# Optimization experiments

Measured on AMD Instinct MI355X. Metric: run time of the kernel, lower is better.

The kernel has to match this reference:

```python
import jax, jax.numpy as jnp
import numpy as np

N_WIRES = 12
N_LAYERS = 3
DIM = 2 ** N_WIRES
BATCH = 512


def _rot_matrix(a, b, c):
    """Fused U = RZ(c) @ RY(b) @ RX(a) as a 2x2 complex64 matrix."""
    ca, sa = jnp.cos(a * 0.5), jnp.sin(a * 0.5)
    cb, sb = jnp.cos(b * 0.5), jnp.sin(b * 0.5)
    ec = jnp.exp(-0.5j * c)  # e^{-i c/2}
    zero = jnp.zeros_like(ec)
    RX = jnp.stack([jnp.stack([ca + 0j, -1j * sa]),
                    jnp.stack([-1j * sa, ca + 0j])]).astype(jnp.complex64)
    RY = jnp.stack([jnp.stack([cb, -sb]),
                    jnp.stack([sb, cb])]).astype(jnp.complex64)
    RZ = jnp.stack([jnp.stack([ec, zero]),
                    jnp.stack([zero, jnp.conj(ec)])]).astype(jnp.complex64)
    return RZ @ RY @ RX


def _apply_1q(psi, U, wire):
    B = psi.shape[0]
    dl, dr = 2 ** wire, 2 ** (N_WIRES - wire - 1)
    s = psi.reshape(B, dl, 2, dr)
    s = jnp.einsum('ij,bljr->blir', U, s)
    return s.reshape(B, DIM)


def _apply_cnot_adjacent(psi, wire):
    # CNOT(control=wire, target=wire+1): permute (10 <-> 11) on the joint axis
    B = psi.shape[0]
    dl, dr = 2 ** wire, 2 ** (N_WIRES - wire - 2)
    s = psi.reshape(B, dl, 4, dr)
    s = jnp.take(s, jnp.array([0, 1, 3, 2]), axis=2)
    return s.reshape(B, DIM)


def _circuit(state_batch, weights):
    psi = state_batch.astype(jnp.complex64)  # QubitStateVector init
    for l in range(N_LAYERS):
        for w in range(N_WIRES):
            U = _rot_matrix(weights[l, w, 0], weights[l, w, 1], weights[l, w, 2])
            psi = _apply_1q(psi, U, w)
        for w in range(N_WIRES - 1):  # 'cnot' chain entanglement
            psi = _apply_cnot_adjacent(psi, w)
    B = state_batch.shape[0]
    probs = (psi.real ** 2 + psi.imag ** 2).reshape((B,) + (2,) * N_WIRES)
    feats = []
    for w in range(N_WIRES):  # <Z_w> = p(0) - p(1)
        axes = tuple(a for a in range(1, N_WIRES + 1) if a != w + 1)
        p = probs.sum(axis=axes)  # (B, 2)
        feats.append(p[:, 0] - p[:, 1])
    return jnp.stack(feats, axis=-1)  # (B, N_WIRES)


def setup_inputs() -> dict:
    key = jax.random.key(0)
    k1, k2, k3, k4 = jax.random.split(key, 4)
    state = jax.random.normal(k1, (BATCH, DIM), dtype=jnp.float32)
    state = state / jnp.linalg.norm(state, axis=-1, keepdims=True)  # valid quantum states
    weights = jax.random.uniform(k2, (N_LAYERS, N_WIRES, 3), dtype=jnp.float32,
                                 minval=0.0, maxval=2.0 * np.pi)
    head_w = jax.random.normal(k3, (1, N_WIRES), dtype=jnp.float32) / np.sqrt(N_WIRES)
    head_b = jax.random.normal(k4, (1,), dtype=jnp.float32) * 0.01
    return {"state_batch": state, "weights": weights, "head_w": head_w, "head_b": head_b}


def reference(state_batch, weights, head_w, head_b):
    feats = _circuit(state_batch, weights)          # (B, N_WIRES) PauliZ expvals
    out = feats @ head_w.T + head_b                 # Linear(num_wires, 1)
    return out[:, 0]                                # squeeze(-1) -> (B,)
```

## Files before the change

kernel.cpp:

```cpp
#include <hip/hip_runtime.h>


namespace {

typedef float v2f __attribute__((ext_vector_type(2)));

constexpr int N_WIRES  = 12;
constexpr int DIM      = 1 << N_WIRES;
constexpr int THREADS  = 256;
constexpr int PER      = 16;
constexpr int NGATES   = 36;
constexpr int PADC     = 4606;

__device__ __forceinline__ v2f cmul(v2f u, v2f p) {
    v2f d;
    asm("v_pk_mul_f32 %0, %1, %2 op_sel_hi:[1,0]"
        : "=v"(d) : "v"(p), "v"(u));
    asm("v_pk_fma_f32 %0, %1, %2, %0 op_sel:[1,1,0] op_sel_hi:[0,1,1] neg_lo:[0,1,0]"
        : "+v"(d) : "v"(p), "v"(u));
    return d;
}
__device__ __forceinline__ void cfma(v2f& d, v2f u, v2f p) {
    asm("v_pk_fma_f32 %0, %1, %2, %0 op_sel_hi:[1,0,1]"
        : "+v"(d) : "v"(p), "v"(u));
    asm("v_pk_fma_f32 %0, %1, %2, %0 op_sel:[1,1,0] op_sel_hi:[0,1,1] neg_lo:[0,1,0]"
        : "+v"(d) : "v"(p), "v"(u));
}

__device__ __forceinline__ void apply4(v2f amp[PER], const v2f (*Um)[4], int gbase)
{
    #pragma unroll
    for (int gg = 0; gg < 4; ++gg) {
        const v2f u00 = Um[gbase + gg][0];
        const v2f u01 = Um[gbase + gg][1];
        const v2f u10 = Um[gbase + gg][2];
        const v2f u11 = Um[gbase + gg][3];
        const int st = 8 >> gg;
        #pragma unroll
        for (int k0 = 0; k0 < PER; ++k0) {
            if (k0 & st) continue;
            const int k1 = k0 | st;
            const v2f p = amp[k0], q = amp[k1];
            v2f np = cmul(u00, p); cfma(np, u01, q);
            v2f nq = cmul(u10, p); cfma(nq, u11, q);
            amp[k0] = np;
            amp[k1] = nq;
        }
    }
}

__global__ __launch_bounds__(THREADS, 4)
void qcirc_kernel(const float* __restrict__ state,
                  const float* __restrict__ weights,
                  const float* __restrict__ head_w,
                  const float* __restrict__ head_b,
                  float* __restrict__ out)
{
    __shared__ __align__(16) v2f buf[PADC];
    __shared__ __align__(16) v2f Umat[NGATES][4];
    __shared__ float redbuf[THREADS / 64];

    const int t = threadIdx.x;
    const int b = blockIdx.x;

    if (t < NGATES) {
        const float* wp = weights + t * 3;
        float ha = 0.5f * wp[0], hb = 0.5f * wp[1], hc = 0.5f * wp[2];
        float ca = cosf(ha), sa = sinf(ha);
        float cb = cosf(hb), sb = sinf(hb);
        float ecr = cosf(hc), eci = -sinf(hc);
        float t0 = cb * ca, t1 = sb * sa, t2 = sb * ca, t3 = cb * sa;
        float u00r =  ecr * t0 - eci * t1;
        float u00i =  ecr * t1 + eci * t0;
        float u10r =  ecr * t2 - eci * t3;
        float u10i = -ecr * t3 - eci * t2;
        Umat[t][0] = (v2f){ u00r,  u00i};
        Umat[t][1] = (v2f){-u10r,  u10i};
        Umat[t][2] = (v2f){ u10r,  u10i};
        Umat[t][3] = (v2f){ u00r, -u00i};
    }

    const int T  = t >> 4, u = t & 15;
    const int bA = 18 * T + u;
    const int bB = 288 * T + u;
    const int bC = 18 * t;
    const int tb  = t ^ (t >> 1);
    const int tbx = tb ^ 128;
    const int pb0 = 18 * (tb  >> 4) + (tb  & 15);
    const int pb1 = 18 * (tbx >> 4) + (tbx & 15);

    float hw[N_WIRES];
    #pragma unroll
    for (int w = 0; w < N_WIRES; ++w) hw[w] = head_w[w];
    int it = t ^ (t >> 1); it ^= it >> 2; it ^= it >> 4;
    float chi = 0.f;
    #pragma unroll
    for (int w = 0; w < 8; ++w)
        chi += ((it >> (7 - w)) & 1) ? -hw[w] : hw[w];
    const int parfill = (__popc(t) & 1) ? 0xF : 0;

    v2f amp[PER];
    {
        const float* sp = state + (size_t)b * DIM;
        #pragma unroll
        for (int k = 0; k < PER; ++k)
            amp[k] = (v2f){sp[(k << 8) | t], 0.f};
    }
    __syncthreads();

    #pragma unroll
    for (int l = 0; l < 3; ++l) {
        const int gb = l * 12;
        if (l > 0) {
            #pragma unroll
            for (int k = 0; k < PER; ++k) {
                const int g = k ^ (k >> 1);
                amp[k] = buf[((k & 1) ? pb1 : pb0) + 288 * g];
            }
            __syncthreads();
        }

        apply4(amp, Umat, gb + 0);
        #pragma unroll
        for (int k = 0; k < PER; ++k) buf[bA + 288 * k] = amp[k];
        __syncthreads();

        #pragma unroll
        for (int k = 0; k < PER; ++k) amp[k] = buf[bB + 18 * k];
        apply4(amp, Umat, gb + 4);
        #pragma unroll
        for (int k = 0; k < PER; ++k) buf[bB + 18 * k] = amp[k];
        __syncthreads();

        {
            const float4* r = reinterpret_cast<const float4*>(&buf[bC]);
            #pragma unroll
            for (int k = 0; k < PER / 2; ++k) {
                float4 v = r[k];
                amp[2 * k]     = (v2f){v.x, v.y};
                amp[2 * k + 1] = (v2f){v.z, v.w};
            }
        }
        apply4(amp, Umat, gb + 8);
        if (l < 2) {
            float4* w = reinterpret_cast<float4*>(&buf[bC]);
            #pragma unroll
            for (int k = 0; k < PER / 2; ++k)
                w[k] = make_float4(amp[2 * k].x, amp[2 * k].y,
                                   amp[2 * k + 1].x, amp[2 * k + 1].y);
            __syncthreads();
        }
    }

    float acc = 0.f;
    #pragma unroll
    for (int k = 0; k < PER; ++k) {
        int ml = (k ^ (k >> 1)); ml ^= ml >> 2; ml ^= parfill;
        float c = chi;
        c += ((ml >> 3) & 1) ? -hw[8]  : hw[8];
        c += ((ml >> 2) & 1) ? -hw[9]  : hw[9];
        c += ((ml >> 1) & 1) ? -hw[10] : hw[10];
        c += ( ml       & 1) ? -hw[11] : hw[11];
        float p = amp[k].x * amp[k].x + amp[k].y * amp[k].y;
        acc += p * c;
    }

    #pragma unroll
    for (int off = 32; off > 0; off >>= 1)
        acc += __shfl_down(acc, off, 64);
    if ((t & 63) == 0) redbuf[t >> 6] = acc;
    __syncthreads();
    if (t == 0) {
        float s = 0.f;
        #pragma unroll
        for (int q = 0; q < THREADS / 64; ++q) s += redbuf[q];
        out[b] = s + head_b[0];
    }
}

}

extern "C" void kernel_launch(void* const* d_in, const int* in_sizes, int n_in,
                              void* d_out, int out_size, void* d_ws, size_t ws_size,
                              hipStream_t stream)
{
    const float* state   = (const float*)d_in[0];
    const float* weights = (const float*)d_in[1];
    const float* head_w  = (const float*)d_in[2];
    const float* head_b  = (const float*)d_in[3];
    float* out = (float*)d_out;

    const int batch = in_sizes[0] / DIM;
    qcirc_kernel<<<batch, THREADS, 0, stream>>>(state, weights, head_w, head_b, out);
}
```

Measured before the change: 76.14 us.

## Use 512 threads with 8 amplitudes each and double-buffered LDS

Doubles the thread count per block to 512, so each thread holds 8 amplitudes instead of 16. Each layer now runs four passes of three gates through shared memory instead of three passes of four. The shared buffer is doubled so that consecutive passes alternate between two buffers, which removes one barrier per layer. The aim is more wavefronts to hide latency and fewer registers per thread, at the cost of an extra LDS exchange pass per layer and twice the LDS footprint per block.

Measured after the change: 78.21 us. 2.7% more time.

```diff
diff --git a/kernel.cpp b/kernel.cpp
--- a/kernel.cpp
+++ b/kernel.cpp
@@ -7,8 +7,8 @@
 
 constexpr int N_WIRES  = 12;
 constexpr int DIM      = 1 << N_WIRES;
-constexpr int THREADS  = 256;
-constexpr int PER      = 16;
+constexpr int THREADS  = 512;
+constexpr int PER      = 8;
 constexpr int NGATES   = 36;
 constexpr int PADC     = 4606;
 
@@ -27,15 +27,15 @@
         : "+v"(d) : "v"(p), "v"(u));
 }
 
-__device__ __forceinline__ void apply4(v2f amp[PER], const v2f (*Um)[4], int gbase)
+__device__ __forceinline__ void apply3(v2f amp[PER], const v2f (*Um)[4], int gbase)
 {
     #pragma unroll
-    for (int gg = 0; gg < 4; ++gg) {
+    for (int gg = 0; gg < 3; ++gg) {
         const v2f u00 = Um[gbase + gg][0];
         const v2f u01 = Um[gbase + gg][1];
         const v2f u10 = Um[gbase + gg][2];
         const v2f u11 = Um[gbase + gg][3];
-        const int st = 8 >> gg;
+        const int st = 4 >> gg;
         #pragma unroll
         for (int k0 = 0; k0 < PER; ++k0) {
             if (k0 & st) continue;
@@ -56,7 +56,7 @@
                   const float* __restrict__ head_b,
                   float* __restrict__ out)
 {
-    __shared__ __align__(16) v2f buf[PADC];
+    __shared__ __align__(16) v2f buf[2][PADC];
     __shared__ __align__(16) v2f Umat[NGATES][4];
     __shared__ float redbuf[THREADS / 64];
 
@@ -80,31 +80,37 @@
         Umat[t][3] = (v2f){ u00r, -u00i};
     }
 
-    const int T  = t >> 4, u = t & 15;
-    const int bA = 18 * T + u;
-    const int bB = 288 * T + u;
-    const int bC = 18 * t;
-    const int tb  = t ^ (t >> 1);
-    const int tbx = tb ^ 128;
-    const int pb0 = 18 * (tb  >> 4) + (tb  & 15);
-    const int pb1 = 18 * (tbx >> 4) + (tbx & 15);
+    const int bP0 = 18 * (t >> 4) + (t & 15);
+    const int bP1 = 576 * (t >> 6) + 18 * ((t >> 4) & 3) + (t & 15);
+    const int bP2 = 72 * (t >> 3) + (t & 7);
+    const int bP3 = 18 * (t >> 1) + 8 * (t & 1);
+
+    const int gt = t ^ (t >> 1);
+    const int gl = gt & 15, gh = gt >> 4;
+    int fg[PER];
+    {
+        const int KT[8] = {0, 3, 6, 5, 12, 15, 10, 9};
+        #pragma unroll
+        for (int k = 0; k < PER; ++k)
+            fg[k] = 18 * ((KT[k] << 4) ^ gh) + gl;
+    }
 
     float hw[N_WIRES];
     #pragma unroll
     for (int w = 0; w < N_WIRES; ++w) hw[w] = head_w[w];
-    int it = t ^ (t >> 1); it ^= it >> 2; it ^= it >> 4;
+    int it = t ^ (t >> 1); it ^= it >> 2; it ^= it >> 4; it ^= it >> 8;
     float chi = 0.f;
     #pragma unroll
-    for (int w = 0; w < 8; ++w)
-        chi += ((it >> (7 - w)) & 1) ? -hw[w] : hw[w];
-    const int parfill = (__popc(t) & 1) ? 0xF : 0;
+    for (int w = 0; w < 9; ++w)
+        chi += ((it >> (8 - w)) & 1) ? -hw[w] : hw[w];
+    const int parfill = (__popc(t) & 1) ? 7 : 0;
 
     v2f amp[PER];
     {
         const float* sp = state + (size_t)b * DIM;
         #pragma unroll
         for (int k = 0; k < PER; ++k)
-            amp[k] = (v2f){sp[(k << 8) | t], 0.f};
+            amp[k] = (v2f){sp[(k << 9) | t], 0.f};
     }
     __syncthreads();
 
@@ -113,51 +119,59 @@
         const int gb = l * 12;
         if (l > 0) {
             #pragma unroll
-            for (int k = 0; k < PER; ++k) {
-                const int g = k ^ (k >> 1);
-                amp[k] = buf[((k & 1) ? pb1 : pb0) + 288 * g];
+            for (int k = 0; k < PER; ++k) amp[k] = buf[1][fg[k]];
+        }
+
+        apply3(amp, Umat, gb + 0);
+        #pragma unroll
+        for (int k = 0; k < PER; ++k) buf[0][bP0 + 576 * k] = amp[k];
+        __syncthreads();
+
+        #pragma unroll
+        for (int k = 0; k < PER; ++k) amp[k] = buf[0][bP1 + 72 * k];
+        apply3(amp, Umat, gb + 3);
+        #pragma unroll
+        for (int k = 0; k < PER; ++k) buf[1][bP1 + 72 * k] = amp[k];
+        __syncthreads();
+
+        #pragma unroll
+        for (int k = 0; k < PER; ++k) {
+            const int o2 = 18 * (k >> 1) + 8 * (k & 1);
+            amp[k] = buf[1][bP2 + o2];
+        }
+        apply3(amp, Umat, gb + 6);
+        #pragma unroll
+        for (int k = 0; k < PER; ++k) {
+            const int o2 = 18 * (k >> 1) + 8 * (k & 1);
+            buf[0][bP2 + o2] = amp[k];
+        }
+        __syncthreads();
+
+        {
+            const float4* r = reinterpret_cast<const float4*>(&buf[0][bP3]);
+            #pragma unroll
+            for (int j = 0; j < PER / 2; ++j) {
+                float4 v = r[j];
+                amp[2 * j]     = (v2f){v.x, v.y};
+                amp[2 * j + 1] = (v2f){v.z, v.w};
             }
+        }
+        apply3(amp, Umat, gb + 9);
+        if (l < 2) {
+            float4* w = reinterpret_cast<float4*>(&buf[1][bP3]);
+            #pragma unroll
+            for (int j = 0; j < PER / 2; ++j)
+                w[j] = make_float4(amp[2 * j].x, amp[2 * j].y,
+                                   amp[2 * j + 1].x, amp[2 * j + 1].y);
             __syncthreads();
         }
-
-        apply4(amp, Umat, gb + 0);
-        #pragma unroll
-        for (int k = 0; k < PER; ++k) buf[bA + 288 * k] = amp[k];
-        __syncthreads();
-
-        #pragma unroll
-        for (int k = 0; k < PER; ++k) amp[k] = buf[bB + 18 * k];
-        apply4(amp, Umat, gb + 4);
-        #pragma unroll
-        for (int k = 0; k < PER; ++k) buf[bB + 18 * k] = amp[k];
-        __syncthreads();
-
-        {
-            const float4* r = reinterpret_cast<const float4*>(&buf[bC]);
-            #pragma unroll
-            for (int k = 0; k < PER / 2; ++k) {
-                float4 v = r[k];
-                amp[2 * k]     = (v2f){v.x, v.y};
-                amp[2 * k + 1] = (v2f){v.z, v.w};
-            }
-        }
-        apply4(amp, Umat, gb + 8);
-        if (l < 2) {
-            float4* w = reinterpret_cast<float4*>(&buf[bC]);
-            #pragma unroll
-            for (int k = 0; k < PER / 2; ++k)
-                w[k] = make_float4(amp[2 * k].x, amp[2 * k].y,
-                                   amp[2 * k + 1].x, amp[2 * k + 1].y);
-            __syncthreads();
-        }
     }
 
     float acc = 0.f;
     #pragma unroll
     for (int k = 0; k < PER; ++k) {
-        int ml = (k ^ (k >> 1)); ml ^= ml >> 2; ml ^= parfill;
+        const int ml = (k ^ (k >> 1) ^ (k >> 2)) ^ parfill;
         float c = chi;
-        c += ((ml >> 3) & 1) ? -hw[8]  : hw[8];
         c += ((ml >> 2) & 1) ? -hw[9]  : hw[9];
         c += ((ml >> 1) & 1) ? -hw[10] : hw[10];
         c += ( ml       & 1) ? -hw[11] : hw[11];
```

## Run each state on a single wavefront holding 64 amplitudes per lane

Applied to the files above, without the earlier changes.

Switches from 256-thread blocks with 16 amplitudes per thread to 64-thread single-wavefront blocks with 64 amplitudes per lane. Six gates are applied per register pass with only two LDS transposes per layer, and the block-wide __syncthreads barriers become s_waitcnt waits. The final reduction is restructured into per-bit partial sums, and the cross-wave LDS reduction is removed. The trade-off is far higher register pressure (128+ VGPRs for amplitudes, risking spills) and fewer waves per CU for latency hiding.

Result: slower. 249.4 us (+227.6%).

```diff
diff --git a/kernel.cpp b/kernel.cpp
--- a/kernel.cpp
+++ b/kernel.cpp
@@ -5,12 +5,14 @@
 
 typedef float v2f __attribute__((ext_vector_type(2)));
 
-constexpr int N_WIRES  = 12;
-constexpr int DIM      = 1 << N_WIRES;
-constexpr int THREADS  = 256;
-constexpr int PER      = 16;
-constexpr int NGATES   = 36;
-constexpr int PADC     = 4606;
+constexpr int N_WIRES = 12;
+constexpr int DIM     = 1 << N_WIRES;
+constexpr int PER     = 64;
+constexpr int NG      = 36;
+
+__host__ __device__ constexpr int ig6(int x) {
+    int y = x; y ^= y >> 1; y ^= y >> 2; y ^= y >> 4; return y & 63;
+}
 
 __device__ __forceinline__ v2f cmul(v2f u, v2f p) {
     v2f d;
@@ -27,44 +29,21 @@
         : "+v"(d) : "v"(p), "v"(u));
 }
 
-__device__ __forceinline__ void apply4(v2f amp[PER], const v2f (*Um)[4], int gbase)
-{
-    #pragma unroll
-    for (int gg = 0; gg < 4; ++gg) {
-        const v2f u00 = Um[gbase + gg][0];
-        const v2f u01 = Um[gbase + gg][1];
-        const v2f u10 = Um[gbase + gg][2];
-        const v2f u11 = Um[gbase + gg][3];
-        const int st = 8 >> gg;
-        #pragma unroll
-        for (int k0 = 0; k0 < PER; ++k0) {
-            if (k0 & st) continue;
-            const int k1 = k0 | st;
-            const v2f p = amp[k0], q = amp[k1];
-            v2f np = cmul(u00, p); cfma(np, u01, q);
-            v2f nq = cmul(u10, p); cfma(nq, u11, q);
-            amp[k0] = np;
-            amp[k1] = nq;
-        }
-    }
-}
-
-__global__ __launch_bounds__(THREADS, 4)
+__global__ __launch_bounds__(64, 1)
 void qcirc_kernel(const float* __restrict__ state,
                   const float* __restrict__ weights,
                   const float* __restrict__ head_w,
                   const float* __restrict__ head_b,
                   float* __restrict__ out)
 {
-    __shared__ __align__(16) v2f buf[PADC];
-    __shared__ __align__(16) v2f Umat[NGATES][4];
-    __shared__ float redbuf[THREADS / 64];
+    __shared__ __align__(16) v2f buf[65 * 64];
+    __shared__ __align__(16) v2f Um[NG][4];
 
-    const int t = threadIdx.x;
+    const int L = threadIdx.x;
     const int b = blockIdx.x;
 
-    if (t < NGATES) {
-        const float* wp = weights + t * 3;
+    if (L < NG) {
+        const float* wp = weights + L * 3;
         float ha = 0.5f * wp[0], hb = 0.5f * wp[1], hc = 0.5f * wp[2];
         float ca = cosf(ha), sa = sinf(ha);
         float cb = cosf(hb), sb = sinf(hb);
@@ -74,108 +53,104 @@
         float u00i =  ecr * t1 + eci * t0;
         float u10r =  ecr * t2 - eci * t3;
         float u10i = -ecr * t3 - eci * t2;
-        Umat[t][0] = (v2f){ u00r,  u00i};
-        Umat[t][1] = (v2f){-u10r,  u10i};
-        Umat[t][2] = (v2f){ u10r,  u10i};
-        Umat[t][3] = (v2f){ u00r, -u00i};
+        Um[L][0] = (v2f){ u00r,  u00i};
+        Um[L][1] = (v2f){-u10r,  u10i};
+        Um[L][2] = (v2f){ u10r,  u10i};
+        Um[L][3] = (v2f){ u00r, -u00i};
     }
 
-    const int T  = t >> 4, u = t & 15;
-    const int bA = 18 * T + u;
-    const int bB = 288 * T + u;
-    const int bC = 18 * t;
-    const int tb  = t ^ (t >> 1);
-    const int tbx = tb ^ 128;
-    const int pb0 = 18 * (tb  >> 4) + (tb  & 15);
-    const int pb1 = 18 * (tbx >> 4) + (tbx & 15);
+    v2f amp[PER];
+    {
+        const float* sp = state + (size_t)b * DIM + L;
+        #pragma unroll
+        for (int k = 0; k < PER; ++k)
+            amp[k] = (v2f){sp[k << 6], 0.f};
+    }
+
+    const int gL  = L ^ (L >> 1);
+    const int gb0 = 65 * gL;
+    const int gb1 = 65 * (gL ^ 32);
+
+    asm volatile("s_waitcnt lgkmcnt(0)" ::: "memory");
+
+    int gi = 0;
+    #pragma unroll 1
+    for (int l = 0; l < 3; ++l) {
+        #pragma unroll 1
+        for (int rep = 0; rep < 2; ++rep) {
+            #pragma unroll
+            for (int gg = 0; gg < 6; ++gg) {
+                const v2f u00 = Um[gi + gg][0];
+                const v2f u01 = Um[gi + gg][1];
+                const v2f u10 = Um[gi + gg][2];
+                const v2f u11 = Um[gi + gg][3];
+                const int st = 32 >> gg;
+                #pragma unroll
+                for (int k0 = 0; k0 < PER; ++k0) {
+                    if (k0 & st) continue;
+                    const int k1 = k0 | st;
+                    const v2f p = amp[k0], q = amp[k1];
+                    v2f np = cmul(u00, p); cfma(np, u01, q);
+                    v2f nq = cmul(u10, p); cfma(nq, u11, q);
+                    amp[k0] = np;
+                    amp[k1] = nq;
+                }
+            }
+            gi += 6;
+            if (rep == 0) {
+                #pragma unroll
+                for (int k = 0; k < PER; ++k) buf[65 * L + k] = amp[k];
+                asm volatile("s_waitcnt lgkmcnt(0)" ::: "memory");
+                #pragma unroll
+                for (int k = 0; k < PER; ++k) amp[k] = buf[L + 65 * k];
+            }
+        }
+        if (l < 2) {
+            #pragma unroll
+            for (int k = 0; k < PER; ++k) buf[L + 65 * k] = amp[k];
+            asm volatile("s_waitcnt lgkmcnt(0)" ::: "memory");
+            #pragma unroll
+            for (int k = 0; k < PER; ++k) {
+                const int gk = (k ^ (k >> 1)) & 63;
+                amp[k] = buf[((k & 1) ? gb1 : gb0) + gk];
+            }
+            asm volatile("s_waitcnt lgkmcnt(0)" ::: "memory");
+        }
+    }
 
     float hw[N_WIRES];
     #pragma unroll
     for (int w = 0; w < N_WIRES; ++w) hw[w] = head_w[w];
-    int it = t ^ (t >> 1); it ^= it >> 2; it ^= it >> 4;
+
+    float P = 0.f, T0 = 0.f, T1 = 0.f, T2 = 0.f, T3 = 0.f, T4 = 0.f, T5 = 0.f;
+    #pragma unroll
+    for (int k = 0; k < PER; ++k) {
+        const float p = amp[k].x * amp[k].x + amp[k].y * amp[k].y;
+        P += p;
+        constexpr auto m = 0;  (void)m;
+        const int mg = ig6(k);
+        if (mg & 32) T0 -= p; else T0 += p;
+        if (mg & 16) T1 -= p; else T1 += p;
+        if (mg &  8) T2 -= p; else T2 += p;
+        if (mg &  4) T3 -= p; else T3 += p;
+        if (mg &  2) T4 -= p; else T4 += p;
+        if (mg &  1) T5 -= p; else T5 += p;
+    }
+    float Q = hw[6] * T0 + hw[7] * T1 + hw[8] * T2
+            + hw[9] * T3 + hw[10] * T4 + hw[11] * T5;
+
+    int iL = L; iL ^= iL >> 1; iL ^= iL >> 2; iL ^= iL >> 4;
     float chi = 0.f;
     #pragma unroll
-    for (int w = 0; w < 8; ++w)
-        chi += ((it >> (7 - w)) & 1) ? -hw[w] : hw[w];
-    const int parfill = (__popc(t) & 1) ? 0xF : 0;
+    for (int w = 0; w < 6; ++w)
+        chi += ((iL >> (5 - w)) & 1) ? -hw[w] : hw[w];
 
-    v2f amp[PER];
-    {
-        const float* sp = state + (size_t)b * DIM;
-        #pragma unroll
-        for (int k = 0; k < PER; ++k)
-            amp[k] = (v2f){sp[(k << 8) | t], 0.f};
-    }
-    __syncthreads();
-
-    #pragma unroll
-    for (int l = 0; l < 3; ++l) {
-        const int gb = l * 12;
-        if (l > 0) {
-            #pragma unroll
-            for (int k = 0; k < PER; ++k) {
-                const int g = k ^ (k >> 1);
-                amp[k] = buf[((k & 1) ? pb1 : pb0) + 288 * g];
-            }
-            __syncthreads();
-        }
-
-        apply4(amp, Umat, gb + 0);
-        #pragma unroll
-        for (int k = 0; k < PER; ++k) buf[bA + 288 * k] = amp[k];
-        __syncthreads();
-
-        #pragma unroll
-        for (int k = 0; k < PER; ++k) amp[k] = buf[bB + 18 * k];
-        apply4(amp, Umat, gb + 4);
-        #pragma unroll
-        for (int k = 0; k < PER; ++k) buf[bB + 18 * k] = amp[k];
-        __syncthreads();
-
-        {
-            const float4* r = reinterpret_cast<const float4*>(&buf[bC]);
-            #pragma unroll
-            for (int k = 0; k < PER / 2; ++k) {
-                float4 v = r[k];
-                amp[2 * k]     = (v2f){v.x, v.y};
-                amp[2 * k + 1] = (v2f){v.z, v.w};
-            }
-        }
-        apply4(amp, Umat, gb + 8);
-        if (l < 2) {
-            float4* w = reinterpret_cast<float4*>(&buf[bC]);
-            #pragma unroll
-            for (int k = 0; k < PER / 2; ++k)
-                w[k] = make_float4(amp[2 * k].x, amp[2 * k].y,
-                                   amp[2 * k + 1].x, amp[2 * k + 1].y);
-            __syncthreads();
-        }
-    }
-
-    float acc = 0.f;
-    #pragma unroll
-    for (int k = 0; k < PER; ++k) {
-        int ml = (k ^ (k >> 1)); ml ^= ml >> 2; ml ^= parfill;
-        float c = chi;
-        c += ((ml >> 3) & 1) ? -hw[8]  : hw[8];
-        c += ((ml >> 2) & 1) ? -hw[9]  : hw[9];
-        c += ((ml >> 1) & 1) ? -hw[10] : hw[10];
-        c += ( ml       & 1) ? -hw[11] : hw[11];
-        float p = amp[k].x * amp[k].x + amp[k].y * amp[k].y;
-        acc += p * c;
-    }
+    float acc = chi * P + ((__popc(L) & 1) ? -Q : Q);
 
     #pragma unroll
     for (int off = 32; off > 0; off >>= 1)
         acc += __shfl_down(acc, off, 64);
-    if ((t & 63) == 0) redbuf[t >> 6] = acc;
-    __syncthreads();
-    if (t == 0) {
-        float s = 0.f;
-        #pragma unroll
-        for (int q = 0; q < THREADS / 64; ++q) s += redbuf[q];
-        out[b] = s + head_b[0];
-    }
+    if (L == 0) out[b] = acc + head_b[0];
 }
 
 }
@@ -191,5 +166,5 @@
     float* out = (float*)d_out;
 
     const int batch = in_sizes[0] / DIM;
-    qcirc_kernel<<<batch, THREADS, 0, stream>>>(state, weights, head_w, head_b, out);
+    qcirc_kernel<<<batch, 64, 0, stream>>>(state, weights, head_w, head_b, out);
 }
```

## Use wavefront shuffles for low wires and fuse cross-wave gate pairs into LDS exchange

Applied to the files above, without the earlier changes.

Restructures the per-layer data movement. Gates on six of the wires are applied through __shfl_xor butterflies inside each wavefront instead of an LDS transpose round. The two gates whose wire index lives across waves are merged into a single 4-term combination computed while reading from a double-buffered LDS array, which cuts barrier count and LDS round trips per layer. The readout is reformulated as per-thread signed partial sums. The changes also reduce launch_bounds occupancy to 2 and stop unrolling the layer loop, trading LDS traffic and barriers for more shuffle and ALU work and higher register pressure.

New measurement: 83.19 us. 9.2% more time.

```diff
diff --git a/kernel.cpp b/kernel.cpp
--- a/kernel.cpp
+++ b/kernel.cpp
@@ -5,12 +5,9 @@
 
 typedef float v2f __attribute__((ext_vector_type(2)));
 
-constexpr int N_WIRES  = 12;
-constexpr int DIM      = 1 << N_WIRES;
-constexpr int THREADS  = 256;
-constexpr int PER      = 16;
-constexpr int NGATES   = 36;
-constexpr int PADC     = 4606;
+constexpr int DIM  = 4096;
+constexpr int NG   = 36;
+constexpr int PADA = 4606;
 
 __device__ __forceinline__ v2f cmul(v2f u, v2f p) {
     v2f d;
@@ -27,17 +24,17 @@
         : "+v"(d) : "v"(p), "v"(u));
 }
 
-__device__ __forceinline__ void apply4(v2f amp[PER], const v2f (*Um)[4], int gbase)
+__device__ __forceinline__ void gates4(v2f amp[16], const v2f (*Um)[4], int gb)
 {
     #pragma unroll
     for (int gg = 0; gg < 4; ++gg) {
-        const v2f u00 = Um[gbase + gg][0];
-        const v2f u01 = Um[gbase + gg][1];
-        const v2f u10 = Um[gbase + gg][2];
-        const v2f u11 = Um[gbase + gg][3];
+        const v2f u00 = Um[gb + gg][0];
+        const v2f u01 = Um[gb + gg][1];
+        const v2f u10 = Um[gb + gg][2];
+        const v2f u11 = Um[gb + gg][3];
         const int st = 8 >> gg;
         #pragma unroll
-        for (int k0 = 0; k0 < PER; ++k0) {
+        for (int k0 = 0; k0 < 16; ++k0) {
             if (k0 & st) continue;
             const int k1 = k0 | st;
             const v2f p = amp[k0], q = amp[k1];
@@ -49,21 +46,21 @@
     }
 }
 
-__global__ __launch_bounds__(THREADS, 4)
+__global__ __launch_bounds__(256, 2)
 void qcirc_kernel(const float* __restrict__ state,
                   const float* __restrict__ weights,
                   const float* __restrict__ head_w,
                   const float* __restrict__ head_b,
                   float* __restrict__ out)
 {
-    __shared__ __align__(16) v2f buf[PADC];
-    __shared__ __align__(16) v2f Umat[NGATES][4];
-    __shared__ float redbuf[THREADS / 64];
+    __shared__ __align__(16) v2f buf[2][PADA];
+    __shared__ __align__(16) v2f Um[NG][4];
+    __shared__ float redbuf[4];
 
     const int t = threadIdx.x;
     const int b = blockIdx.x;
 
-    if (t < NGATES) {
+    if (t < NG) {
         const float* wp = weights + t * 3;
         float ha = 0.5f * wp[0], hb = 0.5f * wp[1], hc = 0.5f * wp[2];
         float ca = cosf(ha), sa = sinf(ha);
@@ -74,108 +71,146 @@
         float u00i =  ecr * t1 + eci * t0;
         float u10r =  ecr * t2 - eci * t3;
         float u10i = -ecr * t3 - eci * t2;
-        Umat[t][0] = (v2f){ u00r,  u00i};
-        Umat[t][1] = (v2f){-u10r,  u10i};
-        Umat[t][2] = (v2f){ u10r,  u10i};
-        Umat[t][3] = (v2f){ u00r, -u00i};
-    }
-
-    const int T  = t >> 4, u = t & 15;
-    const int bA = 18 * T + u;
-    const int bB = 288 * T + u;
-    const int bC = 18 * t;
-    const int tb  = t ^ (t >> 1);
-    const int tbx = tb ^ 128;
-    const int pb0 = 18 * (tb  >> 4) + (tb  & 15);
-    const int pb1 = 18 * (tbx >> 4) + (tbx & 15);
-
-    float hw[N_WIRES];
-    #pragma unroll
-    for (int w = 0; w < N_WIRES; ++w) hw[w] = head_w[w];
-    int it = t ^ (t >> 1); it ^= it >> 2; it ^= it >> 4;
-    float chi = 0.f;
-    #pragma unroll
-    for (int w = 0; w < 8; ++w)
-        chi += ((it >> (7 - w)) & 1) ? -hw[w] : hw[w];
-    const int parfill = (__popc(t) & 1) ? 0xF : 0;
-
-    v2f amp[PER];
+        Um[t][0] = (v2f){ u00r,  u00i};
+        Um[t][1] = (v2f){-u10r,  u10i};
+        Um[t][2] = (v2f){ u10r,  u10i};
+        Um[t][3] = (v2f){ u00r, -u00i};
+    }
+
+    const int bA    = 18 * (t >> 4) + (t & 15);
+    const int bA64  = 18 * ((t >> 4) ^ 4)  + (t & 15);
+    const int bA128 = 18 * ((t >> 4) ^ 8)  + (t & 15);
+    const int bA192 = 18 * ((t >> 4) ^ 12) + (t & 15);
+    const int gt8 = (t ^ (t >> 1)) & 255;
+    const int pbase = 18 * ((gt8 >> 4) & 3) + (gt8 & 15);
+    const int t7 = (t >> 7) & 1, t6 = (t >> 6) & 1;
+    const int j6 = t6 ^ t7;
+
+    v2f amp[16];
     {
         const float* sp = state + (size_t)b * DIM;
         #pragma unroll
-        for (int k = 0; k < PER; ++k)
+        for (int k = 0; k < 16; ++k)
             amp[k] = (v2f){sp[(k << 8) | t], 0.f};
     }
     __syncthreads();
 
-    #pragma unroll
+    #pragma unroll 1
     for (int l = 0; l < 3; ++l) {
         const int gb = l * 12;
         if (l > 0) {
+            const v2f* src = buf[(l - 1) & 1];
+            const v2f* U4 = Um[gb - 8];
+            const v2f* U5 = Um[gb - 7];
+            const v2f a0  = t7 ? U4[2] : U4[0],  a1  = t7 ? U4[3] : U4[1];
+            const v2f a0p = t7 ? U4[0] : U4[2],  a1p = t7 ? U4[1] : U4[3];
+            const v2f b0  = j6 ? U5[2] : U5[0],  b1  = j6 ? U5[3] : U5[1];
+            const v2f cE00 = cmul(a0,  b0), cE01 = cmul(a0,  b1);
+            const v2f cE10 = cmul(a1,  b0), cE11 = cmul(a1,  b1);
+            const v2f cO00 = cmul(a0p, b0), cO01 = cmul(a0p, b1);
+            const v2f cO10 = cmul(a1p, b0), cO11 = cmul(a1p, b1);
             #pragma unroll
-            for (int k = 0; k < PER; ++k) {
-                const int g = k ^ (k >> 1);
-                amp[k] = buf[((k & 1) ? pb1 : pb0) + 288 * g];
+            for (int k = 0; k < 16; ++k) {
+                const int g4 = k ^ (k >> 1);
+                const v2f* s = src + pbase + 288 * g4;
+                const v2f r00 = s[0], r01 = s[72], r10 = s[144], r11 = s[216];
+                v2f nw;
+                if (k & 1) {
+                    nw = cmul(cO00, r00); cfma(nw, cO01, r01);
+                    cfma(nw, cO10, r10);  cfma(nw, cO11, r11);
+                } else {
+                    nw = cmul(cE00, r00); cfma(nw, cE01, r01);
+                    cfma(nw, cE10, r10);  cfma(nw, cE11, r11);
+                }
+                amp[k] = nw;
             }
-            __syncthreads();
-        }
-
-        apply4(amp, Umat, gb + 0);
-        #pragma unroll
-        for (int k = 0; k < PER; ++k) buf[bA + 288 * k] = amp[k];
+        }
+
+        gates4(amp, Um, gb);
+
+        #pragma unroll
+        for (int w6 = 0; w6 < 6; ++w6) {
+            const v2f* Ug = Um[gb + 6 + w6];
+            const v2f u00 = Ug[0], u01 = Ug[1], u10 = Ug[2], u11 = Ug[3];
+            const int mask = 32 >> w6;
+            const bool bo = (t & mask) != 0;
+            const v2f uA = bo ? u11 : u00;
+            const v2f uB = bo ? u10 : u01;
+            #pragma unroll
+            for (int k = 0; k < 16; ++k) {
+                v2f oth;
+                oth.x = __shfl_xor(amp[k].x, mask, 64);
+                oth.y = __shfl_xor(amp[k].y, mask, 64);
+                v2f nw = cmul(uA, amp[k]);
+                cfma(nw, uB, oth);
+                amp[k] = nw;
+            }
+        }
+
+        {
+            v2f* dst = buf[l & 1];
+            #pragma unroll
+            for (int k = 0; k < 16; ++k) dst[bA + 288 * k] = amp[k];
+        }
         __syncthreads();
-
-        #pragma unroll
-        for (int k = 0; k < PER; ++k) amp[k] = buf[bB + 18 * k];
-        apply4(amp, Umat, gb + 4);
-        #pragma unroll
-        for (int k = 0; k < PER; ++k) buf[bB + 18 * k] = amp[k];
-        __syncthreads();
-
-        {
-            const float4* r = reinterpret_cast<const float4*>(&buf[bC]);
-            #pragma unroll
-            for (int k = 0; k < PER / 2; ++k) {
-                float4 v = r[k];
-                amp[2 * k]     = (v2f){v.x, v.y};
-                amp[2 * k + 1] = (v2f){v.z, v.w};
-            }
-        }
-        apply4(amp, Umat, gb + 8);
-        if (l < 2) {
-            float4* w = reinterpret_cast<float4*>(&buf[bC]);
-            #pragma unroll
-            for (int k = 0; k < PER / 2; ++k)
-                w[k] = make_float4(amp[2 * k].x, amp[2 * k].y,
-                                   amp[2 * k + 1].x, amp[2 * k + 1].y);
-            __syncthreads();
-        }
-    }
-
-    float acc = 0.f;
-    #pragma unroll
-    for (int k = 0; k < PER; ++k) {
-        int ml = (k ^ (k >> 1)); ml ^= ml >> 2; ml ^= parfill;
-        float c = chi;
-        c += ((ml >> 3) & 1) ? -hw[8]  : hw[8];
-        c += ((ml >> 2) & 1) ? -hw[9]  : hw[9];
-        c += ((ml >> 1) & 1) ? -hw[10] : hw[10];
-        c += ( ml       & 1) ? -hw[11] : hw[11];
-        float p = amp[k].x * amp[k].x + amp[k].y * amp[k].y;
-        acc += p * c;
-    }
+    }
+
+    {
+        const v2f* src = buf[0];
+        const v2f* U4 = Um[28];
+        const v2f* U5 = Um[29];
+        const v2f a_own = t7 ? U4[3] : U4[0];
+        const v2f a_oth = t7 ? U4[2] : U4[1];
+        const v2f b_own = t6 ? U5[3] : U5[0];
+        const v2f b_oth = t6 ? U5[2] : U5[1];
+        const v2f c_own = cmul(a_own, b_own);
+        const v2f c_64  = cmul(a_own, b_oth);
+        const v2f c_128 = cmul(a_oth, b_own);
+        const v2f c_192 = cmul(a_oth, b_oth);
+        #pragma unroll
+        for (int k = 0; k < 16; ++k) {
+            const int base = 288 * k;
+            const v2f r64  = src[bA64  + base];
+            const v2f r128 = src[bA128 + base];
+            const v2f r192 = src[bA192 + base];
+            v2f nw = cmul(c_own, amp[k]);
+            cfma(nw, c_64,  r64);
+            cfma(nw, c_128, r128);
+            cfma(nw, c_192, r192);
+            amp[k] = nw;
+        }
+    }
+
+    float hw[12];
+    #pragma unroll
+    for (int w = 0; w < 12; ++w) hw[w] = head_w[w];
+
+    float S0 = 0.f, S1 = 0.f, S2 = 0.f, S3 = 0.f, Sp = 0.f;
+    #pragma unroll
+    for (int k = 0; k < 16; ++k) {
+        const float p = amp[k].x * amp[k].x + amp[k].y * amp[k].y;
+        const int ig4 = (k ^ (k >> 1) ^ (k >> 2) ^ (k >> 3)) & 15;
+        S0 += (ig4 & 8) ? -p : p;
+        S1 += (ig4 & 4) ? -p : p;
+        S2 += (ig4 & 2) ? -p : p;
+        S3 += (ig4 & 1) ? -p : p;
+        Sp += (__popc(k) & 1) ? -p : p;
+    }
+    int ig8 = t ^ (t >> 1); ig8 ^= ig8 >> 2; ig8 ^= ig8 >> 4; ig8 &= 255;
+    float chi = 0.f;
+    #pragma unroll
+    for (int w = 4; w < 12; ++w)
+        chi += ((ig8 >> (11 - w)) & 1) ? -hw[w] : hw[w];
+
+    float acc = hw[0] * S0 + hw[1] * S1 + hw[2] * S2 + hw[3] * S3 + chi * Sp;
 
     #pragma unroll
     for (int off = 32; off > 0; off >>= 1)
         acc += __shfl_down(acc, off, 64);
     if ((t & 63) == 0) redbuf[t >> 6] = acc;
     __syncthreads();
-    if (t == 0) {
-        float s = 0.f;
-        #pragma unroll
-        for (int q = 0; q < THREADS / 64; ++q) s += redbuf[q];
-        out[b] = s + head_b[0];
-    }
+    if (t == 0)
+        out[b] = redbuf[0] + redbuf[1] + redbuf[2] + redbuf[3] + head_b[0];
 }
 
 }
@@ -191,5 +226,5 @@
     float* out = (float*)d_out;
 
     const int batch = in_sizes[0] / DIM;
-    qcirc_kernel<<<batch, THREADS, 0, stream>>>(state, weights, head_w, head_b, out);
-}
+    qcirc_kernel<<<batch, 256, 0, stream>>>(state, weights, head_w, head_b, out);
+}
```
